# Kernel optimization log

Measured on AMD Instinct MI355X. Metric: run time of the kernel, lower is better.

Reference implementation:

```python
import jax, jax.numpy as jnp
import numpy as np
from jax import lax

B, T, I, H, L = 512, 2048, 16, 40, 3

def setup_inputs() -> dict:
    key = jax.random.key(0)
    ks = jax.random.split(key, 4 * L + 3)
    bound = 1.0 / np.sqrt(H)
    u = lambda k, shp: jax.random.uniform(k, shp, jnp.float32, -bound, bound)
    inp = {"x": jax.random.normal(ks[0], (B, T, I), jnp.float32)}
    for l in range(L):
        in_dim = I if l == 0 else H
        inp[f"w_ih{l}"] = u(ks[1 + 4 * l], (H, in_dim))
        inp[f"w_hh{l}"] = u(ks[2 + 4 * l], (H, H))
        inp[f"b_ih{l}"] = u(ks[3 + 4 * l], (H,))
        inp[f"b_hh{l}"] = u(ks[4 + 4 * l], (H,))
    inp["fc_w"] = u(ks[4 * L + 1], (1, H))
    inp["fc_b"] = u(ks[4 * L + 2], (1,))
    return inp

def _rnn_layer(x_seq, w_ih, w_hh, b_ih, b_hh):
    # Precompute input projection as one big GEMM: [B, T, H]
    xp = jnp.einsum('bti,hi->bth', x_seq, w_ih) + b_ih + b_hh
    h0 = jnp.zeros((x_seq.shape[0], w_hh.shape[0]), x_seq.dtype)
    def step(h, xt):  # xt: [B, H]
        h = jnp.tanh(xt + h @ w_hh.T)
        return h, h
    _, ys = lax.scan(step, h0, jnp.swapaxes(xp, 0, 1))  # [T, B, H]
    return jnp.swapaxes(ys, 0, 1)  # [B, T, H]

def reference(x, w_ih0, w_hh0, b_ih0, b_hh0,
              w_ih1, w_hh1, b_ih1, b_hh1,
              w_ih2, w_hh2, b_ih2, b_hh2, fc_w, fc_b):
    # Multi-layer tanh RNN (eval mode: inter-layer and final dropout are identity)
    h = _rnn_layer(x, w_ih0, w_hh0, b_ih0, b_hh0)
    h = _rnn_layer(h, w_ih1, w_hh1, b_ih1, b_hh1)
    h = _rnn_layer(h, w_ih2, w_hh2, b_ih2, b_hh2)
    last = h[:, -1, :]                     # [B, H]
    out = last @ fc_w.T + fc_b             # [B, 1]
    return out[:, 0]                       # [B]
```

## Files before the change

kernel.cpp:

```cpp
#include <hip/hip_runtime.h>
#include <cstddef>
#include <cstdint>

#define B_ 512
#define T_ 2048
#define I_ 16
#define H_ 40

typedef __fp16 half_t;
typedef half_t h2 __attribute__((ext_vector_type(2)));
typedef half_t h8 __attribute__((ext_vector_type(8)));

__device__ __forceinline__ float fast_tanh(float x) {
  float e = __builtin_amdgcn_exp2f(x * 2.8853900817779268f);
  return 1.0f - 2.0f * __builtin_amdgcn_rcpf(e + 1.0f);
}

__device__ __forceinline__ float dot2(h2 a, h2 b, float c) {
#if __has_builtin(__builtin_amdgcn_fdot2)
  return __builtin_amdgcn_fdot2(a, b, c, false);
#else
  return c + (float)a[0] * (float)b[0] + (float)a[1] * (float)b[1];
#endif
}

__device__ __forceinline__ h2 pack2(float lo, float hi) {
#if __has_builtin(__builtin_amdgcn_cvt_pkrtz)
  return __builtin_amdgcn_cvt_pkrtz(lo, hi);
#else
  h2 r; r[0] = (half_t)lo; r[1] = (half_t)hi; return r;
#endif
}

#define PIN(v) asm volatile("" : "+v"(v))

#define LOADW(DST, SRC, STR, N2)                                    \
  _Pragma("unroll") for (int k = 0; k < (N2); ++k) {                \
    DST[k][0] = (half_t)SRC[jr * (STR) + 2 * k];                    \
    DST[k][1] = (half_t)SRC[jr * (STR) + 2 * k + 1];                \
    PIN(DST[k]);                                                    \
  }

#define HD4(Q, W, A0, A1, A2, A3)                                   \
  _Pragma("unroll") for (int m = 0; m < 5; ++m) {                   \
    h2 p0 = {Q[m][0], Q[m][1]}, p1 = {Q[m][2], Q[m][3]};            \
    h2 p2 = {Q[m][4], Q[m][5]}, p3 = {Q[m][6], Q[m][7]};            \
    A0 = dot2(p0, (W)[4 * m + 0], A0);                              \
    A1 = dot2(p1, (W)[4 * m + 1], A1);                              \
    A2 = dot2(p2, (W)[4 * m + 2], A2);                              \
    A3 = dot2(p3, (W)[4 * m + 3], A3);                              \
  }

#define TICK(D0, D1, D2, XH) do {                                   \
  h8 q0[5], q1[5], q2[5];                                           \
  if (D0 || D1) { _Pragma("unroll") for (int m = 0; m < 5; ++m)     \
      q0[m] = ((const h8*)&hb16[0][0])[m]; }                        \
  if (D1 || D2) { _Pragma("unroll") for (int m = 0; m < 5; ++m)     \
      q1[m] = ((const h8*)&hb16[1][0])[m]; }                        \
  if (D2)       { _Pragma("unroll") for (int m = 0; m < 5; ++m)     \
      q2[m] = ((const h8*)&hb16[2][0])[m]; }                        \
  float a0=0.f,a1=0.f,a2=0.f,a3=0.f;                                \
  float b0=0.f,b1=0.f,b2=0.f,b3=0.f;                                \
  float c0=0.f,c1=0.f,c2=0.f,c3=0.f;                                \
  float nh0=0.f, nh1=0.f;                                           \
  if (D0) {                                                         \
    a0 = bias0;                                                     \
    a0=dot2(XH[0],w0i[0],a0); a1=dot2(XH[1],w0i[1],a1);             \
    a2=dot2(XH[2],w0i[2],a2); a3=dot2(XH[3],w0i[3],a3);             \
    a0=dot2(XH[4],w0i[4],a0); a1=dot2(XH[5],w0i[5],a1);             \
    a2=dot2(XH[6],w0i[6],a2); a3=dot2(XH[7],w0i[7],a3);             \
    HD4(q0, w0h, a0,a1,a2,a3)                          \
  }                                                                 \
  if (D1) {                                                         \
    b0 = bias1;                                                     \
    HD4(q0, w1i, b0,b1,b2,b3)                          \
    HD4(q1, w1h, b0,b1,b2,b3)                          \
  }                                                                 \
  if (D2) {                                                         \
    c0 = bias2;                                                     \
    HD4(q1, w2i, c0,c1,c2,c3)                          \
    HD4(q2, w2h, c0,c1,c2,c3)                          \
  }                                                                 \
  if (D0) nh0  = fast_tanh((a0 + a1) + (a2 + a3));                  \
  if (D1) nh1  = fast_tanh((b0 + b1) + (b2 + b3));                  \
  if (D2) nh2v = fast_tanh((c0 + c1) + (c2 + c3));                  \
  if (D0) hb16[0][j] = (half_t)nh0;                                 \
  if (D1) hb16[1][j] = (half_t)nh1;                                 \
  if (D2) hb16[2][j] = (half_t)nh2v;                                \
} while (0)

__device__ __forceinline__ void loadx(h2* xh, const float* __restrict__ p) {
  float4 f0 = ((const float4*)p)[0];
  float4 f1 = ((const float4*)p)[1];
  float4 f2 = ((const float4*)p)[2];
  float4 f3 = ((const float4*)p)[3];
  xh[0] = pack2(f0.x, f0.y); xh[1] = pack2(f0.z, f0.w);
  xh[2] = pack2(f1.x, f1.y); xh[3] = pack2(f1.z, f1.w);
  xh[4] = pack2(f2.x, f2.y); xh[5] = pack2(f2.z, f2.w);
  xh[6] = pack2(f3.x, f3.y); xh[7] = pack2(f3.z, f3.w);
}

__global__ __launch_bounds__(64)
__attribute__((amdgpu_waves_per_eu(1, 1)))
void rnn3_fused(const float* __restrict__ x,
                const float* __restrict__ wih0, const float* __restrict__ whh0,
                const float* __restrict__ bih0, const float* __restrict__ bhh0,
                const float* __restrict__ wih1, const float* __restrict__ whh1,
                const float* __restrict__ b_ih1, const float* __restrict__ bhh1,
                const float* __restrict__ wih2, const float* __restrict__ whh2,
                const float* __restrict__ bih2, const float* __restrict__ bhh2,
                const float* __restrict__ fcw, const float* __restrict__ fcb,
                float* __restrict__ out) {
  const int b = blockIdx.x;
  const int j = threadIdx.x;
  const int jr = (j < H_) ? j : (H_ - 1);

  h2 w0i[I_ / 2], w0h[H_ / 2], w1i[H_ / 2], w1h[H_ / 2], w2i[H_ / 2], w2h[H_ / 2];
  LOADW(w0i, wih0, I_, I_ / 2)
  LOADW(w0h, whh0, H_, H_ / 2)
  LOADW(w1i, wih1, H_, H_ / 2)
  LOADW(w1h, whh1, H_, H_ / 2)
  LOADW(w2i, wih2, H_, H_ / 2)
  LOADW(w2h, whh2, H_, H_ / 2)

  float bias0 = bih0[jr] + bhh0[jr];  PIN(bias0);
  float bias1 = b_ih1[jr] + bhh1[jr]; PIN(bias1);
  float bias2 = bih2[jr] + bhh2[jr];  PIN(bias2);

  __shared__ __align__(16) half_t hb16[3][64];
  hb16[0][j] = (half_t)0.f; hb16[1][j] = (half_t)0.f; hb16[2][j] = (half_t)0.f;
  __syncthreads();

  const float* __restrict__ xb = x + (size_t)b * (T_ * I_);

  h2 xA[8], xB[8];
  loadx(xA, xb);
  loadx(xB, xb + I_);

  float nh2v = 0.f;

  TICK(1, 0, 0, xA);  loadx(xA, xb + 2 * I_);
  TICK(1, 1, 0, xB);  loadx(xB, xb + 3 * I_);

  for (int u = 2; u < T_; u += 2) {
    TICK(1, 1, 1, xA);
    { const int tf = (u + 2 < T_) ? u + 2 : T_ - 1; loadx(xA, xb + (size_t)tf * I_); }
    TICK(1, 1, 1, xB);
    { const int tf = (u + 3 < T_) ? u + 3 : T_ - 1; loadx(xB, xb + (size_t)tf * I_); }
  }

  TICK(0, 1, 1, xA);
  TICK(0, 0, 1, xA);

  const float fw = (j < H_) ? fcw[j] : 0.f;
  float v = nh2v * fw;
#pragma unroll
  for (int off = 32; off > 0; off >>= 1) v += __shfl_down(v, off);
  if (j == 0) out[b] = v + fcb[0];
}

extern "C" void kernel_launch(void* const* d_in, const int* in_sizes, int n_in,
                              void* d_out, int out_size, void* d_ws, size_t ws_size,
                              hipStream_t stream) {
  (void)in_sizes; (void)n_in; (void)d_ws; (void)ws_size; (void)out_size;
  const float* x    = (const float*)d_in[0];
  const float* wih0 = (const float*)d_in[1];
  const float* whh0 = (const float*)d_in[2];
  const float* bih0 = (const float*)d_in[3];
  const float* bhh0 = (const float*)d_in[4];
  const float* wih1 = (const float*)d_in[5];
  const float* whh1 = (const float*)d_in[6];
  const float* bih1 = (const float*)d_in[7];
  const float* bhh1 = (const float*)d_in[8];
  const float* wih2 = (const float*)d_in[9];
  const float* whh2 = (const float*)d_in[10];
  const float* bih2 = (const float*)d_in[11];
  const float* bhh2 = (const float*)d_in[12];
  const float* fcw  = (const float*)d_in[13];
  const float* fcb  = (const float*)d_in[14];
  float* out = (float*)d_out;

  hipLaunchKernelGGL(rnn3_fused, dim3(B_), dim3(64), 0, stream,
                     x, wih0, whh0, bih0, bhh0,
                     wih1, whh1, bih1, bhh1,
                     wih2, whh2, bih2, bhh2,
                     fcw, fcb, out);
}
```

Measured before the change: 1.109 ms.

## Interleave two batch rows per wave and prefetch hidden state from LDS

Each 64-thread block now processes two independent batch sequences, alternating their wavefronted 3-layer ticks so one sequence's LDS reads and dependent math can overlap the other's. Hidden-state vectors are preloaded into registers right after each tick's write instead of at the start of the next tick. The grid halves to 256 blocks, which on a 256-CU part gives one wave per CU instead of two, and register pressure roughly doubles for the q/x buffers.

```diff
diff --git a/kernel.cpp b/kernel.cpp
--- a/kernel.cpp
+++ b/kernel.cpp
@@ -41,24 +41,28 @@
     PIN(DST[k]);                                                    \
   }
 
-#define HD4(Q, W, A0, A1, A2, A3)                                   \
+#define HD4O(Q, OFF, W, A0, A1, A2, A3)                             \
   _Pragma("unroll") for (int m = 0; m < 5; ++m) {                   \
-    h2 p0 = {Q[m][0], Q[m][1]}, p1 = {Q[m][2], Q[m][3]};            \
-    h2 p2 = {Q[m][4], Q[m][5]}, p3 = {Q[m][6], Q[m][7]};            \
+    h2 p0 = {Q[(OFF) + m][0], Q[(OFF) + m][1]};                     \
+    h2 p1 = {Q[(OFF) + m][2], Q[(OFF) + m][3]};                     \
+    h2 p2 = {Q[(OFF) + m][4], Q[(OFF) + m][5]};                     \
+    h2 p3 = {Q[(OFF) + m][6], Q[(OFF) + m][7]};                     \
     A0 = dot2(p0, (W)[4 * m + 0], A0);                              \
     A1 = dot2(p1, (W)[4 * m + 1], A1);                              \
     A2 = dot2(p2, (W)[4 * m + 2], A2);                              \
     A3 = dot2(p3, (W)[4 * m + 3], A3);                              \
   }
 
-#define TICK(D0, D1, D2, XH) do {                                   \
-  h8 q0[5], q1[5], q2[5];                                           \
-  if (D0 || D1) { _Pragma("unroll") for (int m = 0; m < 5; ++m)     \
-      q0[m] = ((const h8*)&hb16[0][0])[m]; }                        \
-  if (D1 || D2) { _Pragma("unroll") for (int m = 0; m < 5; ++m)     \
-      q1[m] = ((const h8*)&hb16[1][0])[m]; }                        \
-  if (D2)       { _Pragma("unroll") for (int m = 0; m < 5; ++m)     \
-      q2[m] = ((const h8*)&hb16[2][0])[m]; }                        \
+#define PRELOADQ(Q, SLAB, N0, N1, N2) do {                          \
+  if (N0) { _Pragma("unroll") for (int m = 0; m < 5; ++m)           \
+      Q[m]      = ((const h8*)&SLAB[0][0])[m]; }                    \
+  if (N1) { _Pragma("unroll") for (int m = 0; m < 5; ++m)           \
+      Q[5 + m]  = ((const h8*)&SLAB[1][0])[m]; }                    \
+  if (N2) { _Pragma("unroll") for (int m = 0; m < 5; ++m)           \
+      Q[10 + m] = ((const h8*)&SLAB[2][0])[m]; }                    \
+} while (0)
+
+#define TICKC(D0, D1, D2, Q, XH, SLAB, NH2) do {                    \
   float a0=0.f,a1=0.f,a2=0.f,a3=0.f;                                \
   float b0=0.f,b1=0.f,b2=0.f,b3=0.f;                                \
   float c0=0.f,c1=0.f,c2=0.f,c3=0.f;                                \
@@ -69,24 +73,24 @@
     a2=dot2(XH[2],w0i[2],a2); a3=dot2(XH[3],w0i[3],a3);             \
     a0=dot2(XH[4],w0i[4],a0); a1=dot2(XH[5],w0i[5],a1);             \
     a2=dot2(XH[6],w0i[6],a2); a3=dot2(XH[7],w0i[7],a3);             \
-    HD4(q0, w0h, a0,a1,a2,a3)                          \
+    HD4O(Q, 0, w0h, a0,a1,a2,a3)                       \
   }                                                                 \
   if (D1) {                                                         \
     b0 = bias1;                                                     \
-    HD4(q0, w1i, b0,b1,b2,b3)                          \
-    HD4(q1, w1h, b0,b1,b2,b3)                          \
+    HD4O(Q, 0, w1i, b0,b1,b2,b3)                       \
+    HD4O(Q, 5, w1h, b0,b1,b2,b3)                       \
   }                                                                 \
   if (D2) {                                                         \
     c0 = bias2;                                                     \
-    HD4(q1, w2i, c0,c1,c2,c3)                          \
-    HD4(q2, w2h, c0,c1,c2,c3)                          \
+    HD4O(Q, 5,  w2i, c0,c1,c2,c3)                      \
+    HD4O(Q, 10, w2h, c0,c1,c2,c3)                      \
   }                                                                 \
-  if (D0) nh0  = fast_tanh((a0 + a1) + (a2 + a3));                  \
-  if (D1) nh1  = fast_tanh((b0 + b1) + (b2 + b3));                  \
-  if (D2) nh2v = fast_tanh((c0 + c1) + (c2 + c3));                  \
-  if (D0) hb16[0][j] = (half_t)nh0;                                 \
-  if (D1) hb16[1][j] = (half_t)nh1;                                 \
-  if (D2) hb16[2][j] = (half_t)nh2v;                                \
+  if (D0) nh0 = fast_tanh((a0 + a1) + (a2 + a3));                   \
+  if (D1) nh1 = fast_tanh((b0 + b1) + (b2 + b3));                   \
+  if (D2) NH2 = fast_tanh((c0 + c1) + (c2 + c3));                   \
+  if (D0) SLAB[0][j] = (half_t)nh0;                                 \
+  if (D1) SLAB[1][j] = (half_t)nh1;                                 \
+  if (D2) SLAB[2][j] = (half_t)NH2;                                 \
 } while (0)
 
 __device__ __forceinline__ void loadx(h2* xh, const float* __restrict__ p) {
@@ -111,7 +115,7 @@
                 const float* __restrict__ bih2, const float* __restrict__ bhh2,
                 const float* __restrict__ fcw, const float* __restrict__ fcb,
                 float* __restrict__ out) {
-  const int b = blockIdx.x;
+  const int b0 = 2 * blockIdx.x;
   const int j = threadIdx.x;
   const int jr = (j < H_) ? j : (H_ - 1);
 
@@ -127,36 +131,61 @@
   float bias1 = b_ih1[jr] + bhh1[jr]; PIN(bias1);
   float bias2 = bih2[jr] + bhh2[jr];  PIN(bias2);
 
-  __shared__ __align__(16) half_t hb16[3][64];
-  hb16[0][j] = (half_t)0.f; hb16[1][j] = (half_t)0.f; hb16[2][j] = (half_t)0.f;
+  __shared__ __align__(16) half_t hsA[3][64];
+  __shared__ __align__(16) half_t hsB[3][64];
+  hsA[0][j] = (half_t)0.f; hsA[1][j] = (half_t)0.f; hsA[2][j] = (half_t)0.f;
+  hsB[0][j] = (half_t)0.f; hsB[1][j] = (half_t)0.f; hsB[2][j] = (half_t)0.f;
   __syncthreads();
 
-  const float* __restrict__ xb = x + (size_t)b * (T_ * I_);
-
-  h2 xA[8], xB[8];
-  loadx(xA, xb);
-  loadx(xB, xb + I_);
-
-  float nh2v = 0.f;
-
-  TICK(1, 0, 0, xA);  loadx(xA, xb + 2 * I_);
-  TICK(1, 1, 0, xB);  loadx(xB, xb + 3 * I_);
+  const float* __restrict__ xp0 = x + (size_t)b0 * (T_ * I_);
+  const float* __restrict__ xp1 = xp0 + (size_t)(T_ * I_);
+
+  h2 xA0[8], xB0[8], xA1[8], xB1[8];
+  loadx(xA0, xp0); loadx(xB0, xp0 + I_);
+  loadx(xA1, xp1); loadx(xB1, xp1 + I_);
+
+  float nh2a = 0.f, nh2b = 0.f;
+  h8 qa[15], qb[15];
+
+  PRELOADQ(qa, hsA, 1, 0, 0);
+  PRELOADQ(qb, hsB, 1, 0, 0);
+
+  TICKC(1,0,0, qa, xA0, hsA, nh2a); PRELOADQ(qa, hsA, 1,1,0); loadx(xA0, xp0 + 2*I_);
+  TICKC(1,0,0, qb, xA1, hsB, nh2b); PRELOADQ(qb, hsB, 1,1,0); loadx(xA1, xp1 + 2*I_);
+  TICKC(1,1,0, qa, xB0, hsA, nh2a); PRELOADQ(qa, hsA, 1,1,1); loadx(xB0, xp0 + 3*I_);
+  TICKC(1,1,0, qb, xB1, hsB, nh2b); PRELOADQ(qb, hsB, 1,1,1); loadx(xB1, xp1 + 3*I_);
 
   for (int u = 2; u < T_; u += 2) {
-    TICK(1, 1, 1, xA);
-    { const int tf = (u + 2 < T_) ? u + 2 : T_ - 1; loadx(xA, xb + (size_t)tf * I_); }
-    TICK(1, 1, 1, xB);
-    { const int tf = (u + 3 < T_) ? u + 3 : T_ - 1; loadx(xB, xb + (size_t)tf * I_); }
-  }
-
-  TICK(0, 1, 1, xA);
-  TICK(0, 0, 1, xA);
+    const int tf0 = (u + 2 < T_) ? u + 2 : T_ - 1;
+    TICKC(1,1,1, qa, xA0, hsA, nh2a); PRELOADQ(qa, hsA, 1,1,1);
+    loadx(xA0, xp0 + (size_t)tf0 * I_);
+    TICKC(1,1,1, qb, xA1, hsB, nh2b); PRELOADQ(qb, hsB, 1,1,1);
+    loadx(xA1, xp1 + (size_t)tf0 * I_);
+    const int tf1 = (u + 3 < T_) ? u + 3 : T_ - 1;
+    TICKC(1,1,1, qa, xB0, hsA, nh2a); PRELOADQ(qa, hsA, 1,1,1);
+    loadx(xB0, xp0 + (size_t)tf1 * I_);
+    TICKC(1,1,1, qb, xB1, hsB, nh2b); PRELOADQ(qb, hsB, 1,1,1);
+    loadx(xB1, xp1 + (size_t)tf1 * I_);
+  }
+
+  TICKC(0,1,1, qa, xA0, hsA, nh2a); PRELOADQ(qa, hsA, 0,1,1);
+  TICKC(0,1,1, qb, xA1, hsB, nh2b); PRELOADQ(qb, hsB, 0,1,1);
+  TICKC(0,0,1, qa, xA0, hsA, nh2a);
+  TICKC(0,0,1, qb, xA1, hsB, nh2b);
 
   const float fw = (j < H_) ? fcw[j] : 0.f;
-  float v = nh2v * fw;
+  float va = nh2a * fw;
+  float vb = nh2b * fw;
 #pragma unroll
-  for (int off = 32; off > 0; off >>= 1) v += __shfl_down(v, off);
-  if (j == 0) out[b] = v + fcb[0];
+  for (int off = 32; off > 0; off >>= 1) {
+    va += __shfl_down(va, off);
+    vb += __shfl_down(vb, off);
+  }
+  if (j == 0) {
+    const float fb = fcb[0];
+    out[b0]     = va + fb;
+    out[b0 + 1] = vb + fb;
+  }
 }
 
 extern "C" void kernel_launch(void* const* d_in, const int* in_sizes, int n_in,
@@ -180,7 +209,7 @@
   const float* fcb  = (const float*)d_in[14];
   float* out = (float*)d_out;
 
-  hipLaunchKernelGGL(rnn3_fused, dim3(B_), dim3(64), 0, stream,
+  hipLaunchKernelGGL(rnn3_fused, dim3(B_ / 2), dim3(64), 0, stream,
                      x, wih0, whh0, bih0, bhh0,
                      wih1, whh1, bih1, bhh1,
                      wih2, whh2, bih2, bhh2,
```

After: 2.348 ms. 112% more time.
